# Kernel tuning notes

Measured on AMD Instinct MI355X. Metric: run time of the kernel, lower is better.

Reference implementation:

```python
import jax, jax.numpy as jnp
import numpy as np

ALPHA = 0.2  # LeakyReLU negative slope


def setup_inputs() -> dict:
    key = jax.random.key(0)
    ks = jax.random.split(key, 8)
    B, N, C = 65536, 35, 64
    return {
        "x_target": jax.random.normal(ks[0], (B, C), dtype=jnp.float32),
        "x_neigh": jax.random.normal(ks[1], (B, N, C), dtype=jnp.float32),
        "align_w": jax.random.normal(ks[2], (C, C), dtype=jnp.float32) * 0.05,
        "align_b": jax.random.normal(ks[3], (C,), dtype=jnp.float32) * 0.05,
        "attn1_w": jax.random.normal(ks[4], (16, 2 * C), dtype=jnp.float32) * 0.05,
        "attn1_b": jax.random.normal(ks[5], (16,), dtype=jnp.float32) * 0.05,
        "attn2_w": jax.random.normal(ks[6], (1, 16), dtype=jnp.float32) * 0.05,
        "attn2_b": jax.random.normal(ks[7], (1,), dtype=jnp.float32) * 0.05,
    }


def reference(x_target, x_neigh, align_w, align_b, attn1_w, attn1_b, attn2_w, attn2_b):
    B, N, _ = x_neigh.shape
    # align: Linear(c_in -> c_out) applied to both target and neighbors
    t = x_target @ align_w.T + align_b                 # [B, C]
    n = jnp.einsum('bnc,dc->bnd', x_neigh, align_w) + align_b  # [B, N, C]
    # GAT attention: concat(target broadcast, neigh) -> MLP(2C->16->1)
    a_input = jnp.concatenate([jnp.broadcast_to(t[:, None, :], n.shape), n], axis=-1)  # [B, N, 2C]
    h = jax.nn.relu(jnp.einsum('bnk,hk->bnh', a_input, attn1_w) + attn1_b)  # [B, N, 16]
    e = jax.nn.leaky_relu(jnp.einsum('bnh,oh->bno', h, attn2_w) + attn2_b, ALPHA)[..., 0]  # [B, N]
    attention = jax.nn.softmax(e, axis=-1)             # [B, N]
    h_prime = jnp.einsum('bn,bnc->bc', attention, n)   # weighted neighbor sum [B, C]
    return jax.nn.elu(h_prime)  # concat=True path
```

## Files before the change

### kernel.cpp

```cpp
#include <hip/hip_runtime.h>
#include <math.h>


#define ALPHA 0.2f
static constexpr int Bn = 65536;
static constexpr int Nn = 35;
static constexpr int Cn = 64;

typedef float v2f __attribute__((ext_vector_type(2)));
typedef float v4f __attribute__((ext_vector_type(4)));

#define DPP_XOR1 0xB1
#define DPP_XOR2 0x4E
#define DPP_HMIR 0x141
#define DPP_MIR  0x140

template<int CTRL>
__device__ __forceinline__ float dpp_mov(float x) {
  int r = __builtin_amdgcn_update_dpp(0, __builtin_bit_cast(int, x), CTRL, 0xF, 0xF, true);
  return __builtin_bit_cast(float, r);
}

__device__ __forceinline__ v2f pk_mul(v2f a, v2f b) {
  v2f d; asm("v_pk_mul_f32 %0, %1, %2" : "=v"(d) : "v"(a), "v"(b)); return d;
}
__device__ __forceinline__ v2f pk_fma(v2f a, v2f b, v2f c) {
  v2f d; asm("v_pk_fma_f32 %0, %1, %2, %3" : "=v"(d) : "v"(a), "v"(b), "v"(c)); return d;
}

__device__ __forceinline__ int perm_h(int pos, int m) {
  int p3 = (pos >> 3) & 1;
  int e  = ((pos >> 2) ^ (pos >> 3)) & 1;
  return (pos ^ m) ^ (e ? 3 : 0) ^ (p3 ? 4 : 0);
}

__device__ __forceinline__ float reduce_scatter16(const float p[16]) {
  float q[8];
#pragma unroll
  for (int j = 0; j < 8; ++j) q[j] = p[2*j] + dpp_mov<DPP_XOR1>(p[2*j+1]);
  float r[4];
#pragma unroll
  for (int j = 0; j < 4; ++j) r[j] = q[2*j] + dpp_mov<DPP_XOR2>(q[2*j+1]);
  float s[2];
#pragma unroll
  for (int j = 0; j < 2; ++j) s[j] = r[2*j] + dpp_mov<DPP_HMIR>(r[2*j+1]);
  return s[0] + dpp_mov<DPP_MIR>(s[1]);
}

__device__ __forceinline__ float row_allreduce_add(float x) {
  x += dpp_mov<DPP_XOR1>(x);
  x += dpp_mov<DPP_XOR2>(x);
  x += dpp_mov<DPP_HMIR>(x);
  x += dpp_mov<DPP_MIR>(x);
  return x;
}

__global__ void gat_prep(const float* __restrict__ align_w, const float* __restrict__ align_b,
                         const float* __restrict__ a1w, const float* __restrict__ a1b,
                         float* __restrict__ wsM, float* __restrict__ wsMt, float* __restrict__ wsKt) {
  int t = blockIdx.x * 256 + threadIdx.x;
  if (t < 1024) {
    int h = t >> 6, c = t & 63;
    float accM = 0.f, accMt = 0.f;
    for (int d = 0; d < 64; ++d) {
      float w = align_w[d * 64 + c];
      accM  += a1w[h * 128 + 64 + d] * w;
      accMt += a1w[h * 128 + d] * w;
    }
    wsM[t] = accM;
    wsMt[t] = accMt;
  }
  if (t < 16) {
    float acc = a1b[t];
    for (int d = 0; d < 64; ++d)
      acc += (a1w[t * 128 + d] + a1w[t * 128 + 64 + d]) * align_b[d];
    wsKt[t] = acc;
  }
}

__global__ void gat_u(const float* __restrict__ xt, const float* __restrict__ wsMt,
                      const float* __restrict__ wsKt, float* __restrict__ u_arr) {
  int gt = blockIdx.x * 256 + threadIdx.x;
  int b = gt >> 4, h = gt & 15;
  const v4f* xr = (const v4f*)(xt + (size_t)b * 64);
  const v4f* Mr = (const v4f*)(wsMt + h * 64);
  float acc = wsKt[h];
#pragma unroll
  for (int j = 0; j < 16; ++j) {
    v4f a = Mr[j], x = xr[j];
    acc += a.x * x.x + a.y * x.y + a.z * x.z + a.w * x.w;
  }
  u_arr[gt] = acc;
}

template<bool PRECOMP_U, int MINWAVES>
__global__ __launch_bounds__(256, MINWAVES) void gat_main(
    const float* __restrict__ x_target, const float* __restrict__ x_neigh,
    const float* __restrict__ align_w, const float* __restrict__ align_b,
    const float* __restrict__ attn2_w, const float* __restrict__ attn2_b,
    const float* __restrict__ wsM, const float* __restrict__ wsMt,
    const float* __restrict__ wsKt, const float* __restrict__ u_arr,
    float* __restrict__ out, int waves_total) {
  __shared__ float W_lds[64 * 65];
  __shared__ float xw_lds[4][64];

  int tid = threadIdx.x;
  for (int idx = tid; idx < 4096; idx += 256) {
    int r = idx >> 6, c = idx & 63;
    W_lds[r * 65 + c] = align_w[idx];
  }
  __syncthreads();

  const int lane = tid & 63, wave = tid >> 6;
  const int m = lane & 15, g = lane >> 4;

  v2f Mlo[16], Mhi[16];
#pragma unroll
  for (int pos = 0; pos < 16; ++pos) {
    int h = perm_h(pos, m);
    v4f Mv = ((const v4f*)(wsM + h * 64))[m];
    Mlo[pos] = __builtin_shufflevector(Mv, Mv, 0, 1);
    Mhi[pos] = __builtin_shufflevector(Mv, Mv, 2, 3);
  }
  const float w2r = attn2_w[m];
  const float b2r = attn2_b[0];
  const float biasr = align_b[lane];
  const int wrow = lane * 65;

  v2f Mtlo[16], Mthi[16];
  float Ktr = 0.f;
  if (!PRECOMP_U) {
#pragma unroll
    for (int pos = 0; pos < 16; ++pos) {
      int h = perm_h(pos, m);
      v4f Mv = ((const v4f*)(wsMt + h * 64))[m];
      Mtlo[pos] = __builtin_shufflevector(Mv, Mv, 0, 1);
      Mthi[pos] = __builtin_shufflevector(Mv, Mv, 2, 3);
    }
    Ktr = wsKt[m];
  }

  const int gw = blockIdx.x * 4 + wave;
  for (int b = gw; b < Bn; b += waves_total) {
    const v4f* xb = (const v4f*)(x_neigh + (size_t)b * Nn * Cn);
    v4f x[9];
#pragma unroll
    for (int k = 0; k < 8; ++k) x[k] = xb[lane + 64 * k];
    {
      v4f z = {0.f, 0.f, 0.f, 0.f};
      if (lane < 48) z = xb[512 + lane];
      x[8] = z;
    }

    float uval;
    if (PRECOMP_U) {
      uval = u_arr[(size_t)b * 16 + m];
    } else {
      v4f xt4 = ((const v4f*)(x_target + (size_t)b * 64))[m];
      v2f xtlo = __builtin_shufflevector(xt4, xt4, 0, 1);
      v2f xthi = __builtin_shufflevector(xt4, xt4, 2, 3);
      float up[16];
#pragma unroll
      for (int pos = 0; pos < 16; ++pos) {
        v2f t = pk_mul(Mtlo[pos], xtlo);
        t = pk_fma(Mthi[pos], xthi, t);
        up[pos] = t.x + t.y;
      }
      uval = reduce_scatter16(up) + Ktr;
    }

    float ex[9];
    float mloc = -1e30f;
#pragma unroll
    for (int k = 0; k < 9; ++k) {
      v2f xlo = __builtin_shufflevector(x[k], x[k], 0, 1);
      v2f xhi = __builtin_shufflevector(x[k], x[k], 2, 3);
      float p[16];
#pragma unroll
      for (int pos = 0; pos < 16; ++pos) {
        v2f t = pk_mul(Mlo[pos], xlo);
        t = pk_fma(Mhi[pos], xhi, t);
        p[pos] = t.x + t.y;
      }
      float P = reduce_scatter16(p);
      float rr = fmaxf(P + uval, 0.f) * w2r;
      float esum = row_allreduce_add(rr) + b2r;
      float e = fmaxf(esum, 0.f) + ALPHA * fminf(esum, 0.f);
      if (k == 8 && g == 3) e = -1e30f;
      ex[k] = e;
      mloc = fmaxf(mloc, e);
    }

    mloc = fmaxf(mloc, __shfl_xor(mloc, 16));
    mloc = fmaxf(mloc, __shfl_xor(mloc, 32));
    float sloc = 0.f;
#pragma unroll
    for (int k = 0; k < 9; ++k) {
      ex[k] = __expf(ex[k] - mloc);
      sloc += ex[k];
    }
    sloc += __shfl_xor(sloc, 16);
    sloc += __shfl_xor(sloc, 32);
    const float rS = 1.f / sloc;

    v4f xw = {0.f, 0.f, 0.f, 0.f};
#pragma unroll
    for (int k = 0; k < 9; ++k) {
      xw.x = fmaf(ex[k], x[k].x, xw.x);
      xw.y = fmaf(ex[k], x[k].y, xw.y);
      xw.z = fmaf(ex[k], x[k].z, xw.z);
      xw.w = fmaf(ex[k], x[k].w, xw.w);
    }
    xw.x += __shfl_xor(xw.x, 16); xw.x += __shfl_xor(xw.x, 32);
    xw.y += __shfl_xor(xw.y, 16); xw.y += __shfl_xor(xw.y, 32);
    xw.z += __shfl_xor(xw.z, 16); xw.z += __shfl_xor(xw.z, 32);
    xw.w += __shfl_xor(xw.w, 16); xw.w += __shfl_xor(xw.w, 32);
    xw *= rS;

    if (g == 0)
      *(v4f*)(&xw_lds[wave][4 * m]) = xw;
    asm volatile("s_waitcnt lgkmcnt(0)" ::: "memory");

    v2f hp2 = {0.f, 0.f};
#pragma unroll
    for (int t = 0; t < 16; ++t) {
      v2f xv0 = *(const v2f*)(&xw_lds[wave][4 * t]);
      v2f xv1 = *(const v2f*)(&xw_lds[wave][4 * t + 2]);
      int a = wrow + 4 * t;
      v2f w0 = { W_lds[a],     W_lds[a + 1] };
      v2f w1 = { W_lds[a + 2], W_lds[a + 3] };
      hp2 = pk_fma(w0, xv0, hp2);
      hp2 = pk_fma(w1, xv1, hp2);
    }
    float hp = biasr + hp2.x + hp2.y;
    float en = __expf(fminf(hp, 0.f)) - 1.f;
    out[(size_t)b * 64 + lane] = hp > 0.f ? hp : en;
  }
}

extern "C" void kernel_launch(void* const* d_in, const int* in_sizes, int n_in,
                              void* d_out, int out_size, void* d_ws, size_t ws_size,
                              hipStream_t stream) {
  const float* x_target = (const float*)d_in[0];
  const float* x_neigh  = (const float*)d_in[1];
  const float* align_w  = (const float*)d_in[2];
  const float* align_b  = (const float*)d_in[3];
  const float* attn1_w  = (const float*)d_in[4];
  const float* attn1_b  = (const float*)d_in[5];
  const float* attn2_w  = (const float*)d_in[6];
  const float* attn2_b  = (const float*)d_in[7];
  float* out = (float*)d_out;

  float* ws = (float*)d_ws;
  float* wsM  = ws;
  float* wsMt = ws + 1024;
  float* wsKt = ws + 2048;
  float* u_arr = ws + 2064;
  size_t need = (2064 + (size_t)Bn * 16) * sizeof(float);
  bool precomp = ws_size >= need;

  gat_prep<<<4, 256, 0, stream>>>(align_w, align_b, attn1_w, attn1_b, wsM, wsMt, wsKt);

  const int blocks = 2048;
  const int waves_total = blocks * 4;
  if (precomp) {
    gat_u<<<(Bn * 16) / 256, 256, 0, stream>>>(x_target, wsMt, wsKt, u_arr);
    gat_main<true, 3><<<blocks, 256, 0, stream>>>(x_target, x_neigh, align_w, align_b,
                                                  attn2_w, attn2_b, wsM, wsMt, wsKt,
                                                  u_arr, out, waves_total);
  } else {
    gat_main<false, 2><<<blocks, 256, 0, stream>>>(x_target, x_neigh, align_w, align_b,
                                                   attn2_w, attn2_b, wsM, wsMt, wsKt,
                                                   u_arr, out, waves_total);
  }
}
```

Before: 821.8 us.

## Prefetch next batch neighbors, fuse online softmax, and project output via DPP reduction

Restructures the per-batch loop to software-pipeline loads: neighbor rows for the next batch are prefetched into rotating registers while the current rows are processed. Softmax becomes a single pass accumulating exp weights and the weighted sum directly, without max subtraction. The output projection uses a pre-permuted W layout in LDS and a DPP reduce-scatter instead of staging xw through LDS. This trades numerical safety of the max-shift and more register pressure for lower load latency and fewer LDS round trips.

```diff
diff --git a/kernel.cpp b/kernel.cpp
--- a/kernel.cpp
+++ b/kernel.cpp
@@ -6,6 +6,7 @@
 static constexpr int Bn = 65536;
 static constexpr int Nn = 35;
 static constexpr int Cn = 64;
+static constexpr int NV4 = Nn * Cn / 4;
 
 typedef float v2f __attribute__((ext_vector_type(2)));
 typedef float v4f __attribute__((ext_vector_type(4)));
@@ -27,6 +28,8 @@
 __device__ __forceinline__ v2f pk_fma(v2f a, v2f b, v2f c) {
   v2f d; asm("v_pk_fma_f32 %0, %1, %2, %3" : "=v"(d) : "v"(a), "v"(b), "v"(c)); return d;
 }
+__device__ __forceinline__ v2f lo2(v4f x) { return __builtin_shufflevector(x, x, 0, 1); }
+__device__ __forceinline__ v2f hi2(v4f x) { return __builtin_shufflevector(x, x, 2, 3); }
 
 __device__ __forceinline__ int perm_h(int pos, int m) {
   int p3 = (pos >> 3) & 1;
@@ -101,13 +104,12 @@
     const float* __restrict__ wsM, const float* __restrict__ wsMt,
     const float* __restrict__ wsKt, const float* __restrict__ u_arr,
     float* __restrict__ out, int waves_total) {
-  __shared__ float W_lds[64 * 65];
-  __shared__ float xw_lds[4][64];
-
+  __shared__ v4f W2[16][64];
   int tid = threadIdx.x;
-  for (int idx = tid; idx < 4096; idx += 256) {
-    int r = idx >> 6, c = idx & 63;
-    W_lds[r * 65 + c] = align_w[idx];
+  for (int idx = tid; idx < 1024; idx += 256) {
+    int pos = idx >> 6, l = idx & 63, mm = l & 15, gg = l >> 4;
+    int row = gg * 16 + perm_h(pos, mm);
+    W2[pos][l] = *(const v4f*)(align_w + row * 64 + 4 * mm);
   }
   __syncthreads();
 
@@ -118,47 +120,45 @@
 #pragma unroll
   for (int pos = 0; pos < 16; ++pos) {
     int h = perm_h(pos, m);
-    v4f Mv = ((const v4f*)(wsM + h * 64))[m];
-    Mlo[pos] = __builtin_shufflevector(Mv, Mv, 0, 1);
-    Mhi[pos] = __builtin_shufflevector(Mv, Mv, 2, 3);
+    v4f Mv = *(const v4f*)(wsM + h * 64 + 4 * m);
+    Mlo[pos] = lo2(Mv); Mhi[pos] = hi2(Mv);
   }
   const float w2r = attn2_w[m];
   const float b2r = attn2_b[0];
   const float biasr = align_b[lane];
-  const int wrow = lane * 65;
 
   v2f Mtlo[16], Mthi[16];
   float Ktr = 0.f;
-  if (!PRECOMP_U) {
+  if constexpr (!PRECOMP_U) {
 #pragma unroll
     for (int pos = 0; pos < 16; ++pos) {
       int h = perm_h(pos, m);
-      v4f Mv = ((const v4f*)(wsMt + h * 64))[m];
-      Mtlo[pos] = __builtin_shufflevector(Mv, Mv, 0, 1);
-      Mthi[pos] = __builtin_shufflevector(Mv, Mv, 2, 3);
+      v4f Mv = *(const v4f*)(wsMt + h * 64 + 4 * m);
+      Mtlo[pos] = lo2(Mv); Mthi[pos] = hi2(Mv);
     }
     Ktr = wsKt[m];
   }
 
-  const int gw = blockIdx.x * 4 + wave;
-  for (int b = gw; b < Bn; b += waves_total) {
-    const v4f* xb = (const v4f*)(x_neigh + (size_t)b * Nn * Cn);
-    v4f x[9];
-#pragma unroll
-    for (int k = 0; k < 8; ++k) x[k] = xb[lane + 64 * k];
-    {
-      v4f z = {0.f, 0.f, 0.f, 0.f};
-      if (lane < 48) z = xb[512 + lane];
-      x[8] = z;
-    }
-
-    float uval;
-    if (PRECOMP_U) {
-      uval = u_arr[(size_t)b * 16 + m];
-    } else {
-      v4f xt4 = ((const v4f*)(x_target + (size_t)b * 64))[m];
-      v2f xtlo = __builtin_shufflevector(xt4, xt4, 0, 1);
-      v2f xthi = __builtin_shufflevector(xt4, xt4, 2, 3);
+  const int stride_b = waves_total;
+  int b = blockIdx.x * 4 + wave;
+  if (b >= Bn) return;
+
+  const v4f* xv = (const v4f*)x_neigh;
+  const size_t LASTV = (size_t)Bn * NV4 - 1;
+
+  const v4f* pc = xv + (size_t)b * NV4 + lane;
+  v4f xq0 = pc[0], xq1 = pc[64], xq2 = pc[128];
+  float u_cur = 0.f;
+  if constexpr (PRECOMP_U) u_cur = u_arr[(size_t)b * 16 + m];
+
+  for (; b < Bn; b += stride_b) {
+    const int bn = b + stride_b;
+    const size_t bno = (size_t)(bn < Bn ? bn : Bn - 1) * NV4;
+    const v4f* pn = xv + bno + lane;
+
+    if constexpr (!PRECOMP_U) {
+      v4f xt4 = *(const v4f*)(x_target + (size_t)b * 64 + 4 * m);
+      v2f xtlo = lo2(xt4), xthi = hi2(xt4);
       float up[16];
 #pragma unroll
       for (int pos = 0; pos < 16; ++pos) {
@@ -166,15 +166,14 @@
         t = pk_fma(Mthi[pos], xthi, t);
         up[pos] = t.x + t.y;
       }
-      uval = reduce_scatter16(up) + Ktr;
-    }
-
-    float ex[9];
-    float mloc = -1e30f;
-#pragma unroll
-    for (int k = 0; k < 9; ++k) {
-      v2f xlo = __builtin_shufflevector(x[k], x[k], 0, 1);
-      v2f xhi = __builtin_shufflevector(x[k], x[k], 2, 3);
+      u_cur = reduce_scatter16(up) + Ktr;
+    }
+
+    float s_acc = 0.f;
+    v4f xw = {0.f, 0.f, 0.f, 0.f};
+
+    auto step = [&](v4f xk, bool mask35) {
+      v2f xlo = lo2(xk), xhi = hi2(xk);
       float p[16];
 #pragma unroll
       for (int pos = 0; pos < 16; ++pos) {
@@ -183,58 +182,60 @@
         p[pos] = t.x + t.y;
       }
       float P = reduce_scatter16(p);
-      float rr = fmaxf(P + uval, 0.f) * w2r;
+      float rr = fmaxf(P + u_cur, 0.f) * w2r;
       float esum = row_allreduce_add(rr) + b2r;
       float e = fmaxf(esum, 0.f) + ALPHA * fminf(esum, 0.f);
-      if (k == 8 && g == 3) e = -1e30f;
-      ex[k] = e;
-      mloc = fmaxf(mloc, e);
-    }
-
-    mloc = fmaxf(mloc, __shfl_xor(mloc, 16));
-    mloc = fmaxf(mloc, __shfl_xor(mloc, 32));
-    float sloc = 0.f;
-#pragma unroll
-    for (int k = 0; k < 9; ++k) {
-      ex[k] = __expf(ex[k] - mloc);
-      sloc += ex[k];
-    }
-    sloc += __shfl_xor(sloc, 16);
-    sloc += __shfl_xor(sloc, 32);
-    const float rS = 1.f / sloc;
-
-    v4f xw = {0.f, 0.f, 0.f, 0.f};
-#pragma unroll
-    for (int k = 0; k < 9; ++k) {
-      xw.x = fmaf(ex[k], x[k].x, xw.x);
-      xw.y = fmaf(ex[k], x[k].y, xw.y);
-      xw.z = fmaf(ex[k], x[k].z, xw.z);
-      xw.w = fmaf(ex[k], x[k].w, xw.w);
-    }
+      float w = __expf(e);
+      if (mask35 && g == 3) w = 0.f;
+      s_acc += w;
+      xw.x = fmaf(w, xk.x, xw.x);
+      xw.y = fmaf(w, xk.y, xw.y);
+      xw.z = fmaf(w, xk.z, xw.z);
+      xw.w = fmaf(w, xk.w, xw.w);
+    };
+
+    { v4f t = xq0; xq0 = pc[192]; step(t, false); }
+    { v4f t = xq1; xq1 = pc[256]; step(t, false); }
+    { v4f t = xq2; xq2 = pc[320]; step(t, false); }
+    { v4f t = xq0; xq0 = pc[384]; step(t, false); }
+    { v4f t = xq1; xq1 = pc[448]; step(t, false); }
+    {
+      v4f t = xq2;
+      size_t idx = (size_t)b * NV4 + 512 + lane;
+      if (idx > LASTV) idx = LASTV;
+      xq2 = xv[idx];
+      step(t, false);
+    }
+    float u_nxt = u_cur;
+    { v4f t = xq0; xq0 = pn[0];   step(t, false); }
+    if constexpr (PRECOMP_U)
+      u_nxt = u_arr[(size_t)(bn < Bn ? bn : Bn - 1) * 16 + m];
+    { v4f t = xq1; xq1 = pn[64];  step(t, false); }
+    { v4f t = xq2; xq2 = pn[128]; step(t, true);  }
+
+    s_acc += __shfl_xor(s_acc, 16); s_acc += __shfl_xor(s_acc, 32);
     xw.x += __shfl_xor(xw.x, 16); xw.x += __shfl_xor(xw.x, 32);
     xw.y += __shfl_xor(xw.y, 16); xw.y += __shfl_xor(xw.y, 32);
     xw.z += __shfl_xor(xw.z, 16); xw.z += __shfl_xor(xw.z, 32);
     xw.w += __shfl_xor(xw.w, 16); xw.w += __shfl_xor(xw.w, 32);
-    xw *= rS;
-
-    if (g == 0)
-      *(v4f*)(&xw_lds[wave][4 * m]) = xw;
-    asm volatile("s_waitcnt lgkmcnt(0)" ::: "memory");
-
-    v2f hp2 = {0.f, 0.f};
-#pragma unroll
-    for (int t = 0; t < 16; ++t) {
-      v2f xv0 = *(const v2f*)(&xw_lds[wave][4 * t]);
-      v2f xv1 = *(const v2f*)(&xw_lds[wave][4 * t + 2]);
-      int a = wrow + 4 * t;
-      v2f w0 = { W_lds[a],     W_lds[a + 1] };
-      v2f w1 = { W_lds[a + 2], W_lds[a + 3] };
-      hp2 = pk_fma(w0, xv0, hp2);
-      hp2 = pk_fma(w1, xv1, hp2);
-    }
-    float hp = biasr + hp2.x + hp2.y;
-    float en = __expf(fminf(hp, 0.f)) - 1.f;
-    out[(size_t)b * 64 + lane] = hp > 0.f ? hp : en;
+    const float rS = 1.f / s_acc;
+    v2f xwlo = { xw.x * rS, xw.y * rS };
+    v2f xwhi = { xw.z * rS, xw.w * rS };
+
+    float q[16];
+#pragma unroll
+    for (int pos = 0; pos < 16; ++pos) {
+      v4f Wv = W2[pos][lane];
+      v2f t = pk_mul(lo2(Wv), xwlo);
+      t = pk_fma(hi2(Wv), xwhi, t);
+      q[pos] = t.x + t.y;
+    }
+    float hp = reduce_scatter16(q) + biasr;
+    float res = hp > 0.f ? hp : (__expf(hp) - 1.f);
+    out[(size_t)b * 64 + lane] = res;
+
+    pc = pn;
+    u_cur = u_nxt;
   }
 }
 
```

Measured after the change: 825.2 us. No clear change (+0.4%).
